# Optimization experiments

Hardware: AMD Instinct MI355X
Metric: run time of the kernel (lower is better)

## Reference

```python
import jax, jax.numpy as jnp
import numpy as np

N_NODES = 50000
N_EDGES = 800000
D = 64
E_DIM = 2
C = 8


def _spline_basis(pseudo, K):
    """Open B-spline basis, degree=1. pseudo: [Ne, E] in [0,1).
    Returns basis B [Ne, S] and flat weight index WI [Ne, S], S = 2**E."""
    E = pseudo.shape[1]
    v = pseudo * (K - 1)
    lo_f = jnp.floor(v)
    frac = v - lo_f
    lo = lo_f.astype(jnp.int32)
    idx = jnp.stack([jnp.clip(lo, 0, K - 1), jnp.clip(lo + 1, 0, K - 1)], axis=-1)  # [Ne,E,2]
    bas = jnp.stack([1.0 - frac, frac], axis=-1)                                   # [Ne,E,2]
    combos = jnp.asarray(
        np.stack(np.meshgrid(*([np.arange(2)] * E), indexing='ij'), -1).reshape(-1, E)
    )  # [S,E]
    d_idx = jnp.arange(E)[None, :]          # broadcast to [S,E]
    B = jnp.prod(bas[:, d_idx, combos], axis=-1)  # [Ne,S]
    stride = (K ** jnp.arange(E)).astype(jnp.int32)  # [E]
    WI = jnp.sum(idx[:, d_idx, combos] * stride[None, None, :], axis=-1)  # [Ne,S]
    return B, WI


def _spline_conv(x, src, dst, pseudo, W, root, bias, K, num_nodes):
    """SplineConv (degree=1, open spline, aggr='mean', root_weight, bias).
    x: [N,Din], W: [K**E, Din, Dout], root: [Din, Dout]."""
    B, WI = _spline_basis(pseudo, K)                 # [Ne,S], [Ne,S]
    Y = jnp.einsum('nd,kdo->nko', x, W)              # [N, K**E, Dout]
    gathered = Y[src[:, None], WI]                   # [Ne, S, Dout]
    m = jnp.einsum('es,eso->eo', B, gathered)        # [Ne, Dout]
    msum = jax.ops.segment_sum(m, dst, num_segments=num_nodes)
    cnt = jax.ops.segment_sum(jnp.ones((m.shape[0], 1), m.dtype), dst, num_segments=num_nodes)
    aggr = msum / jnp.maximum(cnt, 1.0)
    return aggr + x @ root + bias


def setup_inputs() -> dict:
    key = jax.random.key(0)
    ks = jax.random.split(key, 16)
    s = 1.0 / np.sqrt(D)
    return {
        'x': jax.random.normal(ks[0], (N_NODES, D), jnp.float32),
        'edge_index': jax.random.randint(ks[1], (2, N_EDGES), 0, N_NODES, jnp.int32),
        'edge_attr': jax.random.uniform(ks[2], (N_EDGES, E_DIM), jnp.float32),
        'W1': jax.random.normal(ks[3], (3 ** E_DIM, D, D), jnp.float32) * s,
        'root1': jax.random.normal(ks[4], (D, D), jnp.float32) * s,
        'b1': jax.random.normal(ks[5], (D,), jnp.float32) * 0.01,
        'W2': jax.random.normal(ks[6], (5 ** E_DIM, D, D), jnp.float32) * s,
        'root2': jax.random.normal(ks[7], (D, D), jnp.float32) * s,
        'b2': jax.random.normal(ks[8], (D,), jnp.float32) * 0.01,
        'mlp1_w': jax.random.normal(ks[9], (D, D), jnp.float32) * s,
        'mlp1_b': jax.random.normal(ks[10], (D,), jnp.float32) * 0.01,
        'mlp2_w': jax.random.normal(ks[11], (D, C), jnp.float32) * s,
        'mlp2_b': jax.random.normal(ks[12], (C,), jnp.float32) * 0.01,
    }


def reference(x, edge_index, edge_attr, W1, root1, b1, W2, root2, b2,
              mlp1_w, mlp1_b, mlp2_w, mlp2_b):
    N = x.shape[0]
    src, dst = edge_index[0], edge_index[1]
    h = jax.nn.elu(_spline_conv(x, src, dst, edge_attr, W1, root1, b1, 3, N))
    # dropout is identity in eval mode
    h = jax.nn.elu(_spline_conv(h, src, dst, edge_attr, W2, root2, b2, 5, N))
    # task='node', G=0 -> no pooling / no concat
    h = jax.nn.relu(h @ mlp1_w + mlp1_b)
    h = jax.nn.relu(h @ mlp2_w + mlp2_b)
    return h
```

## Files before the change

kernel.cpp:

```cpp
#include <hip/hip_runtime.h>
#include <hip/hip_bf16.h>

typedef __attribute__((ext_vector_type(8))) short short8;
typedef __attribute__((ext_vector_type(4))) float floatx4;
typedef __attribute__((ext_vector_type(16))) float floatx16;

__device__ __forceinline__ unsigned short f2bf(float x) {
  __hip_bfloat16 h = __float2bfloat16(x);
  return __builtin_bit_cast(unsigned short, h);
}
__device__ __forceinline__ float bf2f(unsigned short u) {
  return __builtin_bit_cast(float, (unsigned int)u << 16);
}

__global__ __launch_bounds__(256) void cvt_x_kernel(
    const float* __restrict__ X, unsigned short* __restrict__ Xbf, int n) {
  int i = blockIdx.x * 256 + threadIdx.x;
  if (i < n) Xbf[i] = f2bf(X[i]);
}

__global__ __launch_bounds__(256) void pack_b_kernel(
    const float* __restrict__ W, const float* __restrict__ root,
    unsigned short* __restrict__ Bpk, int K2) {
  int R = (K2 + 1) * 64;
  int total = 64 * R;
  int i = blockIdx.x * 256 + threadIdx.x;
  if (i >= total) return;
  int j = i & 7;
  int lane = (i >> 3) & 63;
  int rest = i >> 9;
  int wv = rest & 3, kc = rest >> 2;
  int o = wv * 16 + (lane & 15);
  int r = kc * 32 + ((lane >> 4) & 3) * 8 + j;
  int k = r >> 6, d = r & 63;
  float v = (k < K2) ? W[(k << 12) + (d << 6) + o] : root[(d << 6) + o];
  Bpk[i] = f2bf(v);
}

__global__ __launch_bounds__(256) void zero_int_kernel(int* __restrict__ p, int n) {
  int i = blockIdx.x * 256 + threadIdx.x;
  if (i < n) p[i] = 0;
}

__global__ __launch_bounds__(256) void hist_kernel(
    const int* __restrict__ dst, int* __restrict__ deg, int nE) {
  int e = blockIdx.x * 256 + threadIdx.x;
  if (e < nE) atomicAdd(&deg[dst[e]], 1);
}

__global__ __launch_bounds__(256) void blocksum_kernel(
    const int* __restrict__ deg, int* __restrict__ partial, int N) {
  __shared__ int s[256];
  int t = threadIdx.x, i = blockIdx.x * 256 + t;
  s[t] = (i < N) ? deg[i] : 0;
  __syncthreads();
  for (int off = 128; off > 0; off >>= 1) {
    if (t < off) s[t] += s[t + off];
    __syncthreads();
  }
  if (t == 0) partial[blockIdx.x] = s[0];
}

__global__ __launch_bounds__(256) void scanpartials_kernel(
    int* __restrict__ partial, int nb) {
  __shared__ int s[256];
  int t = threadIdx.x;
  int v = (t < nb) ? partial[t] : 0;
  s[t] = v;
  __syncthreads();
  for (int off = 1; off < 256; off <<= 1) {
    int x = (t >= off) ? s[t - off] : 0;
    __syncthreads();
    s[t] += x;
    __syncthreads();
  }
  if (t < nb) partial[t] = s[t] - v;
}

__global__ __launch_bounds__(256) void blockscan_kernel(
    const int* __restrict__ deg, const int* __restrict__ partial,
    int* __restrict__ row_start, int* __restrict__ cursor, int N, int nE) {
  __shared__ int s[256];
  int t = threadIdx.x, i = blockIdx.x * 256 + t;
  int v = (i < N) ? deg[i] : 0;
  s[t] = v;
  __syncthreads();
  for (int off = 1; off < 256; off <<= 1) {
    int x = (t >= off) ? s[t - off] : 0;
    __syncthreads();
    s[t] += x;
    __syncthreads();
  }
  if (i < N) {
    int excl = s[t] - v + partial[blockIdx.x];
    row_start[i] = excl;
    cursor[i] = excl;
  }
  if (i == 0) row_start[N] = nE;
}

__global__ __launch_bounds__(256) void scatter_rec_kernel(
    const int* __restrict__ dst, const int* __restrict__ src,
    const float* __restrict__ attr, int* __restrict__ cursor,
    float4* __restrict__ rec3, float4* __restrict__ rec5, int nE) {
  int e = blockIdx.x * 256 + threadIdx.x;
  if (e >= nE) return;
  int pos = atomicAdd(&cursor[dst[e]], 1);
  float2 a = *(const float2*)&attr[2 * e];
  int off = src[e] * 64;
  {
    float u = a.x * 2.f, v = a.y * 2.f;
    int l0 = min((int)u, 1), l1 = min((int)v, 1);
    rec3[pos] = make_float4(u - (float)l0, v - (float)l1,
                            __builtin_bit_cast(float, l0 | (l1 << 8)),
                            __builtin_bit_cast(float, off));
  }
  {
    float u = a.x * 4.f, v = a.y * 4.f;
    int l0 = min((int)u, 3), l1 = min((int)v, 3);
    rec5[pos] = make_float4(u - (float)l0, v - (float)l1,
                            __builtin_bit_cast(float, l0 | (l1 << 8)),
                            __builtin_bit_cast(float, off));
  }
}

template <int K, int K2, int OUTBF>
__global__ __launch_bounds__(256) void spline_layer_kernel(
    const float4* __restrict__ rec, const int* __restrict__ row_start,
    const unsigned short* __restrict__ Xbf, const unsigned short* __restrict__ Bpk,
    const float* __restrict__ bias, void* __restrict__ outv, int N) {
  constexpr int RZ = K2 * 64;
  constexpr int AS = RZ + 8;
  constexpr int NKZ = RZ / 32;
  constexpr int NKC = (K2 + 1) * 2;
  __shared__ unsigned short As[16 * AS];
  const int t = threadIdx.x, w = t >> 6, lane = t & 63;
  const int nodeBase = blockIdx.x * 16;

  const int col = lane & 31, half = lane >> 5;
  const int mi0 = (col < K2) ? (col % K) : -3;
  const int mi1 = (col < K2) ? (col / K) : -3;

  for (int g = 0; g < 4; ++g) {
    const int row = w * 4 + g;
    const int node = nodeBase + row;
    if (node < N) {
      floatx16 d0, d1;
#pragma unroll
      for (int i = 0; i < 16; ++i) { d0[i] = 0.f; d1[i] = 0.f; }

      const int beg = row_start[node], end = row_start[node + 1];
      for (int c0 = beg; c0 < end; c0 += 16) {
        const int m = min(16, end - c0);
        float4 rj[8];
#pragma unroll
        for (int j = 0; j < 8; ++j) {
          int idx = half * 8 + j;
          rj[j] = rec[c0 + min(idx, m - 1)];
          if (idx >= m) rj[j].z = __builtin_bit_cast(float, 0x7F7F);
        }
        short8 A, Blo, Bhi;
#pragma unroll
        for (int j = 0; j < 8; ++j) {
          int lp = __builtin_bit_cast(int, rj[j].z);
          int off = __builtin_bit_cast(int, rj[j].w);
          int l0 = lp & 0xFF, l1 = (lp >> 8) & 0xFF;
          float su = (mi0 == l0) ? (1.f - rj[j].x) : ((mi0 == l0 + 1) ? rj[j].x : 0.f);
          float sv = (mi1 == l1) ? (1.f - rj[j].y) : ((mi1 == l1 + 1) ? rj[j].y : 0.f);
          A[j] = (short)f2bf(su * sv);
          Blo[j] = (short)Xbf[off + col];
          Bhi[j] = (short)Xbf[off + 32 + col];
        }
        d0 = __builtin_amdgcn_mfma_f32_32x32x16_bf16(A, Blo, d0, 0, 0, 0);
        d1 = __builtin_amdgcn_mfma_f32_32x32x16_bf16(A, Bhi, d1, 0, 0, 0);
      }

      const float inv = 1.f / (float)max(end - beg, 1);
#pragma unroll
      for (int reg = 0; reg < 16; ++reg) {
        int r = (reg & 3) + 8 * (reg >> 2) + 4 * half;
        if (r < K2) {
          As[row * AS + r * 64 + col] = f2bf(d0[reg] * inv);
          As[row * AS + r * 64 + 32 + col] = f2bf(d1[reg] * inv);
        }
      }
    } else {
      for (int i = lane; i < RZ; i += 64) As[row * AS + i] = 0;
    }
  }
  __syncthreads();

  const int mrow = lane & 15, q = lane >> 4;
  const int anode = min(nodeBase + mrow, N - 1);
  floatx4 acc = {0.f, 0.f, 0.f, 0.f};
#pragma unroll
  for (int kc = 0; kc < NKC; ++kc) {
    short8 a;
    if (kc < NKZ)
      a = *(const short8*)&As[mrow * AS + kc * 32 + q * 8];
    else
      a = *(const short8*)&Xbf[(size_t)anode * 64 + (kc - NKZ) * 32 + q * 8];
    short8 b = *(const short8*)&Bpk[(((size_t)kc * 4 + w) * 64 + lane) * 8];
    acc = __builtin_amdgcn_mfma_f32_16x16x32_bf16(a, b, acc, 0, 0, 0);
  }

  const int o = w * 16 + mrow;
  const float bv = bias[o];
#pragma unroll
  for (int reg = 0; reg < 4; ++reg) {
    int node = nodeBase + q * 4 + reg;
    if (node < N) {
      float v = acc[reg] + bv;
      v = v > 0.f ? v : (expf(v) - 1.f);
      if (OUTBF)
        ((unsigned short*)outv)[(size_t)node * 64 + o] = f2bf(v);
      else
        ((float*)outv)[(size_t)node * 64 + o] = v;
    }
  }
}

__global__ __launch_bounds__(256) void head_kernel(
    const unsigned short* __restrict__ h2bf, const unsigned short* __restrict__ m1pk,
    const float* __restrict__ m1b, const float* __restrict__ m2w,
    const float* __restrict__ m2b, float* __restrict__ out, int N) {
  __shared__ unsigned short Hs[64 * 72];
  __shared__ unsigned short Ts[64 * 72];
  __shared__ float W2s[512];
  const int t = threadIdx.x, w = t >> 6, lane = t & 63;
  const int n0 = blockIdx.x * 64;

  for (int i = t; i < 512; i += 256) {
    int row = i >> 3, cg = i & 7;
    int n = n0 + row;
    floatx4 val = {0.f, 0.f, 0.f, 0.f};
    if (n < N) val = *(const floatx4*)&h2bf[(size_t)n * 64 + cg * 8];
    *(floatx4*)&Hs[row * 72 + cg * 8] = val;
  }
  for (int i = t; i < 512; i += 256) W2s[i] = m2w[i];
  __syncthreads();

  const int mrow = lane & 15, q = lane >> 4;
  const int o = w * 16 + mrow;
  const float bv = m1b[o];
#pragma unroll
  for (int rg = 0; rg < 4; ++rg) {
    floatx4 acc = {0.f, 0.f, 0.f, 0.f};
#pragma unroll
    for (int kc = 0; kc < 2; ++kc) {
      short8 a = *(const short8*)&Hs[(rg * 16 + mrow) * 72 + kc * 32 + q * 8];
      short8 b = *(const short8*)&m1pk[(((size_t)kc * 4 + w) * 64 + lane) * 8];
      acc = __builtin_amdgcn_mfma_f32_16x16x32_bf16(a, b, acc, 0, 0, 0);
    }
#pragma unroll
    for (int reg = 0; reg < 4; ++reg) {
      int row = rg * 16 + q * 4 + reg;
      float v = acc[reg] + bv;
      Ts[row * 72 + o] = f2bf(v > 0.f ? v : 0.f);
    }
  }
  __syncthreads();

  for (int i = t; i < 512; i += 256) {
    int nl = i >> 3, c = i & 7;
    int n = n0 + nl;
    if (n >= N) continue;
    float s = m2b[c];
    for (int d = 0; d < 64; ++d) s += bf2f(Ts[nl * 72 + d]) * W2s[d * 8 + c];
    out[(size_t)n * 8 + c] = s > 0.f ? s : 0.f;
  }
}

extern "C" void kernel_launch(void* const* d_in, const int* in_sizes, int n_in,
                              void* d_out, int out_size, void* d_ws, size_t ws_size,
                              hipStream_t stream) {
  const float* x     = (const float*)d_in[0];
  const int*   ei    = (const int*)d_in[1];
  const float* attr  = (const float*)d_in[2];
  const float* W1    = (const float*)d_in[3];
  const float* root1 = (const float*)d_in[4];
  const float* b1    = (const float*)d_in[5];
  const float* W2    = (const float*)d_in[6];
  const float* root2 = (const float*)d_in[7];
  const float* b2    = (const float*)d_in[8];
  const float* m1w   = (const float*)d_in[9];
  const float* m1b   = (const float*)d_in[10];
  const float* m2w   = (const float*)d_in[11];
  const float* m2b   = (const float*)d_in[12];

  const int N  = in_sizes[0] / 64;
  const int nE = in_sizes[1] / 2;
  const int* src  = ei;
  const int* dstv = ei + nE;
  float* out = (float*)d_out;

  int* deg       = (int*)d_ws;
  int* row_start = deg + N;
  int* cursor    = row_start + (N + 1);
  int* partial   = cursor + N;
  char* pbase = (char*)(partial + 256);
  pbase = (char*)(((uintptr_t)pbase + 15) & ~(uintptr_t)15);
  float4* rec3 = (float4*)pbase;
  float4* rec5 = rec3 + nE;
  unsigned short* Xbf  = (unsigned short*)(rec5 + nE);
  unsigned short* h1bf = Xbf + (size_t)N * 64;
  unsigned short* h2bf = h1bf + (size_t)N * 64;
  unsigned short* Bpk1 = h2bf + (size_t)N * 64;
  unsigned short* Bpk2 = Bpk1 + 64 * 640;
  unsigned short* m1pk = Bpk2 + 64 * 1664;

  dim3 blk(256);
  int nbN  = (N + 255) / 256;
  int nbE  = (nE + 255) / 256;
  int nbF  = (N + 15) / 16;
  int nbH  = (N + 63) / 64;

  zero_int_kernel<<<nbN, blk, 0, stream>>>(deg, N);
  hist_kernel<<<nbE, blk, 0, stream>>>(dstv, deg, nE);
  blocksum_kernel<<<nbN, blk, 0, stream>>>(deg, partial, N);
  scanpartials_kernel<<<1, blk, 0, stream>>>(partial, nbN);
  blockscan_kernel<<<nbN, blk, 0, stream>>>(deg, partial, row_start, cursor, N, nE);
  scatter_rec_kernel<<<nbE, blk, 0, stream>>>(dstv, src, attr, cursor, rec3, rec5, nE);

  pack_b_kernel<<<(64 * 640 + 255) / 256, blk, 0, stream>>>(W1, root1, Bpk1, 9);
  pack_b_kernel<<<(64 * 1664 + 255) / 256, blk, 0, stream>>>(W2, root2, Bpk2, 25);
  pack_b_kernel<<<(64 * 64 + 255) / 256, blk, 0, stream>>>(m1w, m1w, m1pk, 0);
  cvt_x_kernel<<<(N * 64 + 255) / 256, blk, 0, stream>>>(x, Xbf, N * 64);

  spline_layer_kernel<3, 9, 1><<<nbF, blk, 0, stream>>>(
      rec3, row_start, Xbf, Bpk1, b1, h1bf, N);

  spline_layer_kernel<5, 25, 1><<<nbF, blk, 0, stream>>>(
      rec5, row_start, h1bf, Bpk2, b2, h2bf, N);

  head_kernel<<<nbH, blk, 0, stream>>>(h2bf, m1pk, m1b, m2w, m2b, out, N);
}
```

Measured before the change: 345.5 us.

## Precompute bf16 spline basis coefficients in padded chunked layout during CSR scatter

The CSR build now pads each node's edge segment to a multiple of 16. The scatter kernel computes the bf16 spline basis coefficients for every edge and writes them in a transposed per-chunk layout that matches the MFMA A-operand, plus a separate source-offset array. The spline layer kernels then load A with one vector load per lane instead of recomputing the basis from float4 records, and they no longer need tail masking. The cost is more workspace traffic (16/32 bf16 coefficients per padded edge versus two float4 records), an extra pad kernel, and wasted MFMA work on padded slots.

```diff
diff --git a/kernel.cpp b/kernel.cpp
--- a/kernel.cpp
+++ b/kernel.cpp
@@ -52,7 +52,7 @@
     const int* __restrict__ deg, int* __restrict__ partial, int N) {
   __shared__ int s[256];
   int t = threadIdx.x, i = blockIdx.x * 256 + t;
-  s[t] = (i < N) ? deg[i] : 0;
+  s[t] = (i < N) ? ((deg[i] + 15) & ~15) : 0;
   __syncthreads();
   for (int off = 128; off > 0; off >>= 1) {
     if (t < off) s[t] += s[t + off];
@@ -79,10 +79,10 @@
 
 __global__ __launch_bounds__(256) void blockscan_kernel(
     const int* __restrict__ deg, const int* __restrict__ partial,
-    int* __restrict__ row_start, int* __restrict__ cursor, int N, int nE) {
+    int* __restrict__ prow, int* __restrict__ cursor, int N) {
   __shared__ int s[256];
   int t = threadIdx.x, i = blockIdx.x * 256 + t;
-  int v = (i < N) ? deg[i] : 0;
+  int v = (i < N) ? ((deg[i] + 15) & ~15) : 0;
   s[t] = v;
   __syncthreads();
   for (int off = 1; off < 256; off <<= 1) {
@@ -93,53 +93,84 @@
   }
   if (i < N) {
     int excl = s[t] - v + partial[blockIdx.x];
-    row_start[i] = excl;
+    prow[i] = excl;
     cursor[i] = excl;
-  }
-  if (i == 0) row_start[N] = nE;
-}
-
-__global__ __launch_bounds__(256) void scatter_rec_kernel(
+    if (i == N - 1) prow[N] = excl + v;
+  }
+}
+
+__global__ __launch_bounds__(256) void scatter_coeff_kernel(
     const int* __restrict__ dst, const int* __restrict__ src,
     const float* __restrict__ attr, int* __restrict__ cursor,
-    float4* __restrict__ rec3, float4* __restrict__ rec5, int nE) {
+    int* __restrict__ offs, unsigned short* __restrict__ cT3,
+    unsigned short* __restrict__ cT5, int nE) {
   int e = blockIdx.x * 256 + threadIdx.x;
   if (e >= nE) return;
   int pos = atomicAdd(&cursor[dst[e]], 1);
+  int chunk = pos >> 4, kp = pos & 15;
   float2 a = *(const float2*)&attr[2 * e];
-  int off = src[e] * 64;
+  offs[pos] = src[e] * 64;
   {
     float u = a.x * 2.f, v = a.y * 2.f;
     int l0 = min((int)u, 1), l1 = min((int)v, 1);
-    rec3[pos] = make_float4(u - (float)l0, v - (float)l1,
-                            __builtin_bit_cast(float, l0 | (l1 << 8)),
-                            __builtin_bit_cast(float, off));
+    float f0 = u - (float)l0, f1 = v - (float)l1;
+    for (int col = 0; col < 16; ++col) {
+      int mi0 = (col < 9) ? (col % 3) : -3;
+      int mi1 = (col < 9) ? (col / 3) : -3;
+      float su = (mi0 == l0) ? (1.f - f0) : ((mi0 == l0 + 1) ? f0 : 0.f);
+      float sv = (mi1 == l1) ? (1.f - f1) : ((mi1 == l1 + 1) ? f1 : 0.f);
+      cT3[(size_t)chunk * 256 + col * 16 + kp] = f2bf(su * sv);
+    }
   }
   {
     float u = a.x * 4.f, v = a.y * 4.f;
     int l0 = min((int)u, 3), l1 = min((int)v, 3);
-    rec5[pos] = make_float4(u - (float)l0, v - (float)l1,
-                            __builtin_bit_cast(float, l0 | (l1 << 8)),
-                            __builtin_bit_cast(float, off));
-  }
+    float f0 = u - (float)l0, f1 = v - (float)l1;
+    for (int col = 0; col < 32; ++col) {
+      int mi0 = (col < 25) ? (col % 5) : -3;
+      int mi1 = (col < 25) ? (col / 5) : -3;
+      float su = (mi0 == l0) ? (1.f - f0) : ((mi0 == l0 + 1) ? f0 : 0.f);
+      float sv = (mi1 == l1) ? (1.f - f1) : ((mi1 == l1 + 1) ? f1 : 0.f);
+      cT5[(size_t)chunk * 512 + col * 16 + kp] = f2bf(su * sv);
+    }
+  }
+}
+
+__global__ __launch_bounds__(256) void pad_kernel(
+    const int* __restrict__ deg, const int* __restrict__ prow,
+    int* __restrict__ offs, unsigned short* __restrict__ cT3,
+    unsigned short* __restrict__ cT5, int N) {
+  int i = blockIdx.x * 256 + threadIdx.x;
+  int node = i >> 4, s = i & 15;
+  if (node >= N) return;
+  int d = deg[node];
+  int pd = (d + 15) & ~15;
+  if (d + s >= pd) return;
+  int pos = prow[node] + d + s;
+  int chunk = pos >> 4, kp = pos & 15;
+  offs[pos] = 0;
+  for (int col = 0; col < 16; ++col)
+    cT3[(size_t)chunk * 256 + col * 16 + kp] = 0;
+  for (int col = 0; col < 32; ++col)
+    cT5[(size_t)chunk * 512 + col * 16 + kp] = 0;
 }
 
 template <int K, int K2, int OUTBF>
 __global__ __launch_bounds__(256) void spline_layer_kernel(
-    const float4* __restrict__ rec, const int* __restrict__ row_start,
+    const unsigned short* __restrict__ cT, const int* __restrict__ offs,
+    const int* __restrict__ prow, const int* __restrict__ deg,
     const unsigned short* __restrict__ Xbf, const unsigned short* __restrict__ Bpk,
     const float* __restrict__ bias, void* __restrict__ outv, int N) {
   constexpr int RZ = K2 * 64;
   constexpr int AS = RZ + 8;
   constexpr int NKZ = RZ / 32;
   constexpr int NKC = (K2 + 1) * 2;
+  constexpr int CSTRIDE = (K == 3) ? 256 : 512;
   __shared__ unsigned short As[16 * AS];
   const int t = threadIdx.x, w = t >> 6, lane = t & 63;
   const int nodeBase = blockIdx.x * 16;
 
   const int col = lane & 31, half = lane >> 5;
-  const int mi0 = (col < K2) ? (col % K) : -3;
-  const int mi1 = (col < K2) ? (col / K) : -3;
 
   for (int g = 0; g < 4; ++g) {
     const int row = w * 4 + g;
@@ -149,33 +180,32 @@
 #pragma unroll
       for (int i = 0; i < 16; ++i) { d0[i] = 0.f; d1[i] = 0.f; }
 
-      const int beg = row_start[node], end = row_start[node + 1];
-      for (int c0 = beg; c0 < end; c0 += 16) {
-        const int m = min(16, end - c0);
-        float4 rj[8];
+      const int beg = prow[node], endp = prow[node + 1];
+      for (int c0 = beg; c0 < endp; c0 += 16) {
+        const int chunk = c0 >> 4;
+        short8 A;
+        if (K == 3) {
+          short8 tmp = *(const short8*)&cT[(size_t)chunk * CSTRIDE +
+                                           (col & 15) * 16 + half * 8];
+          short8 zero = {0, 0, 0, 0, 0, 0, 0, 0};
+          A = (col < 16) ? tmp : zero;
+        } else {
+          A = *(const short8*)&cT[(size_t)chunk * CSTRIDE + col * 16 + half * 8];
+        }
+        int offj[8];
+#pragma unroll
+        for (int j = 0; j < 8; ++j) offj[j] = offs[c0 + half * 8 + j];
+        short8 Blo, Bhi;
 #pragma unroll
         for (int j = 0; j < 8; ++j) {
-          int idx = half * 8 + j;
-          rj[j] = rec[c0 + min(idx, m - 1)];
-          if (idx >= m) rj[j].z = __builtin_bit_cast(float, 0x7F7F);
-        }
-        short8 A, Blo, Bhi;
-#pragma unroll
-        for (int j = 0; j < 8; ++j) {
-          int lp = __builtin_bit_cast(int, rj[j].z);
-          int off = __builtin_bit_cast(int, rj[j].w);
-          int l0 = lp & 0xFF, l1 = (lp >> 8) & 0xFF;
-          float su = (mi0 == l0) ? (1.f - rj[j].x) : ((mi0 == l0 + 1) ? rj[j].x : 0.f);
-          float sv = (mi1 == l1) ? (1.f - rj[j].y) : ((mi1 == l1 + 1) ? rj[j].y : 0.f);
-          A[j] = (short)f2bf(su * sv);
-          Blo[j] = (short)Xbf[off + col];
-          Bhi[j] = (short)Xbf[off + 32 + col];
+          Blo[j] = (short)Xbf[offj[j] + col];
+          Bhi[j] = (short)Xbf[offj[j] + 32 + col];
         }
         d0 = __builtin_amdgcn_mfma_f32_32x32x16_bf16(A, Blo, d0, 0, 0, 0);
         d1 = __builtin_amdgcn_mfma_f32_32x32x16_bf16(A, Bhi, d1, 0, 0, 0);
       }
 
-      const float inv = 1.f / (float)max(end - beg, 1);
+      const float inv = 1.f / (float)max(deg[node], 1);
 #pragma unroll
       for (int reg = 0; reg < 16; ++reg) {
         int r = (reg & 3) + 8 * (reg >> 2) + 4 * half;
@@ -294,15 +324,18 @@
   const int* dstv = ei + nE;
   float* out = (float*)d_out;
 
-  int* deg       = (int*)d_ws;
-  int* row_start = deg + N;
-  int* cursor    = row_start + (N + 1);
-  int* partial   = cursor + N;
+  const size_t maxPE = (size_t)nE + 16 * (size_t)N;
+  const size_t maxChunks = maxPE / 16;
+  int* deg     = (int*)d_ws;
+  int* prow    = deg + N;
+  int* cursor  = prow + (N + 1);
+  int* partial = cursor + N;
   char* pbase = (char*)(partial + 256);
   pbase = (char*)(((uintptr_t)pbase + 15) & ~(uintptr_t)15);
-  float4* rec3 = (float4*)pbase;
-  float4* rec5 = rec3 + nE;
-  unsigned short* Xbf  = (unsigned short*)(rec5 + nE);
+  int* offs = (int*)pbase;
+  unsigned short* cT3 = (unsigned short*)(offs + maxPE);
+  unsigned short* cT5 = cT3 + maxChunks * 256;
+  unsigned short* Xbf  = cT5 + maxChunks * 512;
   unsigned short* h1bf = Xbf + (size_t)N * 64;
   unsigned short* h2bf = h1bf + (size_t)N * 64;
   unsigned short* Bpk1 = h2bf + (size_t)N * 64;
@@ -312,6 +345,7 @@
   dim3 blk(256);
   int nbN  = (N + 255) / 256;
   int nbE  = (nE + 255) / 256;
+  int nbP  = (N * 16 + 255) / 256;
   int nbF  = (N + 15) / 16;
   int nbH  = (N + 63) / 64;
 
@@ -319,8 +353,10 @@
   hist_kernel<<<nbE, blk, 0, stream>>>(dstv, deg, nE);
   blocksum_kernel<<<nbN, blk, 0, stream>>>(deg, partial, N);
   scanpartials_kernel<<<1, blk, 0, stream>>>(partial, nbN);
-  blockscan_kernel<<<nbN, blk, 0, stream>>>(deg, partial, row_start, cursor, N, nE);
-  scatter_rec_kernel<<<nbE, blk, 0, stream>>>(dstv, src, attr, cursor, rec3, rec5, nE);
+  blockscan_kernel<<<nbN, blk, 0, stream>>>(deg, partial, prow, cursor, N);
+  scatter_coeff_kernel<<<nbE, blk, 0, stream>>>(dstv, src, attr, cursor,
+                                                offs, cT3, cT5, nE);
+  pad_kernel<<<nbP, blk, 0, stream>>>(deg, prow, offs, cT3, cT5, N);
 
   pack_b_kernel<<<(64 * 640 + 255) / 256, blk, 0, stream>>>(W1, root1, Bpk1, 9);
   pack_b_kernel<<<(64 * 1664 + 255) / 256, blk, 0, stream>>>(W2, root2, Bpk2, 25);
@@ -328,10 +364,10 @@
   cvt_x_kernel<<<(N * 64 + 255) / 256, blk, 0, stream>>>(x, Xbf, N * 64);
 
   spline_layer_kernel<3, 9, 1><<<nbF, blk, 0, stream>>>(
-      rec3, row_start, Xbf, Bpk1, b1, h1bf, N);
+      cT3, offs, prow, deg, Xbf, Bpk1, b1, h1bf, N);
 
   spline_layer_kernel<5, 25, 1><<<nbF, blk, 0, stream>>>(
-      rec5, row_start, h1bf, Bpk2, b2, h2bf, N);
+      cT5, offs, prow, deg, h1bf, Bpk2, b2, h2bf, N);
 
   head_kernel<<<nbH, blk, 0, stream>>>(h2bf, m1pk, m1b, m2w, m2b, out, N);
 }
```

New measurement: 628.7 us. +82.0%, slower.
